# Kernel optimization log

Hardware: AMD Instinct MI355X
Metric: run time of the kernel (lower is better)

Reference implementation:

```python
import jax, jax.numpy as jnp
import numpy as np

B, T, C = 4, 2048, 2048
N_HEAD = 16
HEAD_DIM = C // N_HEAD  # 128
ROPE_BASE = 10000.0


def rope_cache(dim, seq_len, base=ROPE_BASE):
    inv_freq = 1.0 / (base ** (jnp.arange(0, dim, 2, dtype=jnp.float32) / dim))
    t = jnp.arange(seq_len, dtype=jnp.float32)
    freqs = jnp.outer(t, inv_freq)  # [T, dim//2]
    return jnp.cos(freqs), jnp.sin(freqs)


def apply_rope(q, k, cos, sin):
    # q, k: [B, H, T, D], interleaved-pair rotation
    q1, q2 = q[..., 0::2], q[..., 1::2]
    k1, k2 = k[..., 0::2], k[..., 1::2]
    c = cos[None, None, :, :]
    s = sin[None, None, :, :]
    q_rot = jnp.stack([q1 * c - q2 * s, q1 * s + q2 * c], axis=-1).reshape(q.shape)
    k_rot = jnp.stack([k1 * c - k2 * s, k1 * s + k2 * c], axis=-1).reshape(k.shape)
    return q_rot, k_rot


def setup_inputs() -> dict:
    key = jax.random.key(0)
    k1, k2, k3 = jax.random.split(key, 3)
    x = jax.random.normal(k1, (B, T, C), dtype=jnp.float32)
    W_attn = jax.random.normal(k2, (3 * C, C), dtype=jnp.float32) * (1.0 / np.sqrt(C))
    W_proj = jax.random.normal(k3, (C, C), dtype=jnp.float32) * (1.0 / np.sqrt(C))
    return {"x": x, "W_attn": W_attn, "W_proj": W_proj}


def reference(x, W_attn, W_proj):
    Bx, Tx, Cx = x.shape
    qkv = jnp.einsum('btc,fc->btf', x, W_attn)  # [B, T, 3C]
    q, k, v = jnp.split(qkv, 3, axis=-1)
    # [B, H, T, D]
    q = q.reshape(Bx, Tx, N_HEAD, HEAD_DIM).transpose(0, 2, 1, 3)
    k = k.reshape(Bx, Tx, N_HEAD, HEAD_DIM).transpose(0, 2, 1, 3)
    v = v.reshape(Bx, Tx, N_HEAD, HEAD_DIM).transpose(0, 2, 1, 3)
    cos, sin = rope_cache(HEAD_DIM, Tx)
    q, k = apply_rope(q, k, cos, sin)
    scale = 1.0 / np.sqrt(HEAD_DIM)
    scores = jnp.einsum('bhqd,bhkd->bhqk', q, k) * scale
    causal = jnp.tril(jnp.ones((Tx, Tx), dtype=bool))
    scores = jnp.where(causal[None, None, :, :], scores, jnp.finfo(scores.dtype).min)
    attn = jax.nn.softmax(scores, axis=-1)
    y = jnp.einsum('bhqk,bhkd->bhqd', attn, v)
    y = y.transpose(0, 2, 1, 3).reshape(Bx, Tx, Cx)
    return jnp.einsum('btc,fc->btf', y, W_proj)
```

## Files before the change

### kernel.cpp

```cpp
#include <hip/hip_runtime.h>
#include <stdint.h>

#define TT 2048
#define CC 2048
#define NHEAD 16
#define HD 128
#define NB 4
#define MTOT (NB*TT)
#define KD 2048
#define NT 32

typedef __attribute__((ext_vector_type(8))) short bf16x8;
typedef __attribute__((ext_vector_type(4))) float f32x4;
typedef __attribute__((ext_vector_type(16))) float f32x16;
typedef __attribute__((ext_vector_type(4))) unsigned u32x4;

__device__ __forceinline__ unsigned short f2bf(float f) {
  unsigned u = __float_as_uint(f);
  u += 0x7FFF + ((u >> 16) & 1);
  return (unsigned short)(u >> 16);
}
__device__ __forceinline__ float bf2f(unsigned short h) {
  return __uint_as_float(((unsigned)h) << 16);
}

__device__ __forceinline__ void gl_lds16(const unsigned short* g, short* l) {
  __builtin_amdgcn_global_load_lds(
      (const __attribute__((address_space(1))) void*)(g),
      (__attribute__((address_space(3))) void*)(l), 16, 0, 0);
}

#define MFMA16(a, b, c) __builtin_amdgcn_mfma_f32_16x16x32_bf16((a), (b), (c), 0, 0, 0)
#define MFMA32(a, b, c) __builtin_amdgcn_mfma_f32_32x32x16_bf16((a), (b), (c), 0, 0, 0)

#define PRE_MFMA() do { \
  __builtin_amdgcn_s_barrier(); \
  asm volatile("s_waitcnt lgkmcnt(0)" ::: "memory"); \
  __builtin_amdgcn_s_setprio(1); \
} while(0)
#define POST_MFMA() do { \
  __builtin_amdgcn_s_setprio(0); \
  __builtin_amdgcn_s_barrier(); \
  __builtin_amdgcn_sched_barrier(0); \
} while(0)

__global__ void k_f2b(const float* __restrict__ in, unsigned short* __restrict__ out, int n4) {
  int i = blockIdx.x * 256 + threadIdx.x;
  if (i >= n4) return;
  float4 v = reinterpret_cast<const float4*>(in)[i];
  ushort4 o;
  o.x = f2bf(v.x); o.y = f2bf(v.y); o.z = f2bf(v.z); o.w = f2bf(v.w);
  reinterpret_cast<ushort4*>(out)[i] = o;
}

__global__ void k_rope_tab(float* __restrict__ tab) {
  int t = blockIdx.x, i = threadIdx.x;
  double inv = exp2(-(double)i * (13.287712379549449062 / 64.0));
  double ang = (double)t * inv;
  tab[(t*64 + i)*2 + 0] = (float)cos(ang);
  tab[(t*64 + i)*2 + 1] = (float)sin(ang);
}

__device__ __forceinline__ void gemm256_core(
    const unsigned short* __restrict__ Ag,
    const unsigned short* __restrict__ Bg,
    int m0, int n0, short* lds, f32x4 (&acc)[8][4])
{
  const int tid = threadIdx.x;
  const int wid = tid >> 6, lane = tid & 63;
  const int wm = wid >> 2, wn = wid & 3;
  const int r15 = lane & 15, hi4 = lane >> 4;
  const int srow = wid*8 + (lane >> 3);
  const int schunk = (lane & 7) ^ (lane >> 3);

  const f32x4 fz = {0.f, 0.f, 0.f, 0.f};
#pragma unroll
  for (int i = 0; i < 8; i++)
#pragma unroll
    for (int j = 0; j < 4; j++) acc[i][j] = fz;

  int aoff0[8];
#pragma unroll
  for (int mi = 0; mi < 8; mi++) {
    int row = wm*128 + mi*16 + r15;
    aoff0[mi] = row*64 + ((hi4 ^ (row & 7))*8);
  }
  int boff0[4];
#pragma unroll
  for (int ni = 0; ni < 4; ni++) {
    int row = wn*64 + ni*16 + r15;
    boff0[ni] = row*64 + ((hi4 ^ (row & 7))*8);
  }

#define STAGE(G, L, GROW0, KT) do { \
    gl_lds16((G) + (size_t)((GROW0) + srow)*KD + (KT) + schunk*8, (L) + wid*512); \
    gl_lds16((G) + (size_t)((GROW0) + 64 + srow)*KD + (KT) + schunk*8, (L) + 4096 + wid*512); \
  } while(0)

  STAGE(Ag, lds,                        m0,       0);
  STAGE(Ag, lds + 8192,                 m0 + 128, 0);
  STAGE(Bg, lds + 32768,                n0,       0);
  STAGE(Bg, lds + 32768 + 8192,         n0 + 128, 0);
  STAGE(Bg, lds + 32768 + 16384,        n0,       64);
  STAGE(Bg, lds + 32768 + 16384 + 8192, n0 + 128, 64);
  asm volatile("s_waitcnt vmcnt(4)" ::: "memory");
  __builtin_amdgcn_s_barrier();
  __builtin_amdgcn_sched_barrier(0);

#pragma unroll 1
  for (int t = 0; t < NT; t++) {
    const int db = t & 1;
    short* Ab = lds + db*16384;
    short* Bb = lds + 32768 + db*16384;
    short* An = lds + (db ^ 1)*16384;
    const int kt = t*64;
    const bool stA = (t < NT - 1);
    const bool stB = (t < NT - 2);

    bf16x8 a[8], b[4][2];
#pragma unroll
    for (int mi = 0; mi < 8; mi++)
      a[mi] = *reinterpret_cast<const bf16x8*>(Ab + aoff0[mi]);
#pragma unroll
    for (int ni = 0; ni < 4; ni++) {
      b[ni][0] = *reinterpret_cast<const bf16x8*>(Bb + boff0[ni]);
      b[ni][1] = *reinterpret_cast<const bf16x8*>(Bb + (boff0[ni] ^ 32));
    }
    if (stA) {
      STAGE(Ag, An,        m0,       kt + 64);
      STAGE(Ag, An + 8192, m0 + 128, kt + 64);
    }
    PRE_MFMA();
#pragma unroll
    for (int mi = 0; mi < 8; mi++)
#pragma unroll
      for (int ni = 0; ni < 4; ni++)
        acc[mi][ni] = MFMA16(a[mi], b[ni][0], acc[mi][ni]);
    POST_MFMA();

#pragma unroll
    for (int mi = 0; mi < 8; mi++)
      a[mi] = *reinterpret_cast<const bf16x8*>(Ab + (aoff0[mi] ^ 32));
    if (stB) {
      STAGE(Bg, Bb,        n0,       kt + 128);
      STAGE(Bg, Bb + 8192, n0 + 128, kt + 128);
    }
    if (t >= NT - 2) asm volatile("s_waitcnt vmcnt(0)" ::: "memory");
    else             asm volatile("s_waitcnt vmcnt(4)" ::: "memory");
    PRE_MFMA();
#pragma unroll
    for (int mi = 0; mi < 8; mi++)
#pragma unroll
      for (int ni = 0; ni < 4; ni++)
        acc[mi][ni] = MFMA16(a[mi], b[ni][1], acc[mi][ni]);
    POST_MFMA();
  }
#undef STAGE
}

__global__ __launch_bounds__(512, 2) void k_qkv(
    const unsigned short* __restrict__ xb,
    const unsigned short* __restrict__ wab,
    unsigned short* __restrict__ qr,
    unsigned short* __restrict__ kr,
    unsigned short* __restrict__ vt)
{
  __shared__ __align__(16) short lds[65536];
  f32x4 acc[8][4];
  int bid = blockIdx.x;
  int swz = (bid & 7)*96 + (bid >> 3);
  int m0 = (swz / 24)*256, n0 = (swz % 24)*256;
  gemm256_core(xb, wab, m0, n0, lds, acc);

  int tid = threadIdx.x, wid = tid >> 6, lane = tid & 63;
  int wm = wid >> 2, wn = wid & 3, r15 = lane & 15, hi4 = lane >> 4;
  int nw0 = n0 + wn*64;
  int which = nw0 >> 11;
  int h = (nw0 & 2047) >> 7;
#pragma unroll
  for (int mi = 0; mi < 8; mi++) {
    int m_base = m0 + wm*128 + mi*16 + hi4*4;
    int b = m_base >> 11;
    int t0 = m_base & (TT - 1);
#pragma unroll
    for (int ni = 0; ni < 4; ni++) {
      int d = (nw0 & 127) + ni*16 + r15;
      if (which == 2) {
        ushort4 pv;
        pv.x = f2bf(acc[mi][ni][0]); pv.y = f2bf(acc[mi][ni][1]);
        pv.z = f2bf(acc[mi][ni][2]); pv.w = f2bf(acc[mi][ni][3]);
        *reinterpret_cast<ushort4*>(vt + ((size_t)((b*NHEAD + h)*HD + d))*TT + t0) = pv;
      } else {
        unsigned short* dst = (which == 0) ? qr : kr;
        size_t base = ((size_t)(b*NHEAD + h)*TT + t0)*HD + d;
#pragma unroll
        for (int r = 0; r < 4; r++) dst[base + (size_t)r*HD] = f2bf(acc[mi][ni][r]);
      }
    }
  }
}

__global__ __launch_bounds__(512, 2) void k_proj(
    const unsigned short* __restrict__ yb,
    const unsigned short* __restrict__ wpb,
    float* __restrict__ out)
{
  __shared__ __align__(16) short lds[65536];
  f32x4 acc[8][4];
  int bid = blockIdx.x;
  int swz = (bid & 7)*32 + (bid >> 3);
  int m0 = (swz / 8)*256, n0 = (swz % 8)*256;
  gemm256_core(yb, wpb, m0, n0, lds, acc);

  int tid = threadIdx.x, wid = tid >> 6, lane = tid & 63;
  int wm = wid >> 2, wn = wid & 3, r15 = lane & 15, hi4 = lane >> 4;
  int nw0 = n0 + wn*64;
#pragma unroll
  for (int mi = 0; mi < 8; mi++) {
    int m = m0 + wm*128 + mi*16 + hi4*4;
#pragma unroll
    for (int ni = 0; ni < 4; ni++) {
      int n = nw0 + ni*16 + r15;
#pragma unroll
      for (int r = 0; r < 4; r++)
        out[(size_t)(m + r)*CC + n] = acc[mi][ni][r];
    }
  }
}

__global__ void k_rope_apply(unsigned int* __restrict__ q32, unsigned int* __restrict__ k32,
                             const float* __restrict__ tab) {
  int i = blockIdx.x * 256 + threadIdx.x;
  int ii = i & 63;
  int t = (i >> 6) & (TT - 1);
  float c = tab[(t*64 + ii)*2], s = tab[(t*64 + ii)*2 + 1];
  unsigned qv = q32[i];
  float q1 = bf2f((unsigned short)qv), q2 = bf2f((unsigned short)(qv >> 16));
  unsigned short lo = f2bf(q1*c - q2*s), hi = f2bf(q1*s + q2*c);
  q32[i] = (unsigned)lo | ((unsigned)hi << 16);
  unsigned kv = k32[i];
  float k1 = bf2f((unsigned short)kv), k2 = bf2f((unsigned short)(kv >> 16));
  lo = f2bf(k1*c - k2*s); hi = f2bf(k1*s + k2*c);
  k32[i] = (unsigned)lo | ((unsigned)hi << 16);
}

__global__ __launch_bounds__(256, 1) void k_attn(
    const unsigned short* __restrict__ qr,
    const unsigned short* __restrict__ kr,
    const unsigned short* __restrict__ vt,
    unsigned short* __restrict__ yb)
{
  __shared__ __align__(16) short Ks[2][64*128];
  __shared__ __align__(16) short Vs[2][128*64];
  __shared__ float alds[4][32];
  int bid = blockIdx.x;
  int bh = bid & 63, pr = bid >> 6;
  int tid = threadIdx.x, w = tid >> 6, lane = tid & 63;
  int l31 = lane & 31, hi = lane >> 5;
  const unsigned short* qg = qr + (size_t)bh*TT*HD;
  const unsigned short* kg = kr + (size_t)bh*TT*HD;
  const unsigned short* vg = vt + (size_t)bh*HD*TT;
  const float scale = 0.08838834764831845f;
  int b = bh >> 4, h = bh & 15;

  int ksoff[4], vsoff[4];
#pragma unroll
  for (int i = 0; i < 4; i++) {
    int rK = (w*4 + i)*4 + (lane >> 4);
    int cK = (lane & 15) ^ (rK & 7);
    ksoff[i] = rK*HD + cK*8;
    int dV = (w*4 + i)*8 + (lane >> 3);
    int cV = (lane & 7) ^ (dV & 7);
    vsoff[i] = dV*TT + cV*8;
  }

#define STAGE_KV(BUF, KV0) do { \
    _Pragma("unroll") \
    for (int i_ = 0; i_ < 4; i_++) { \
      gl_lds16(kg + (size_t)(KV0)*HD + ksoff[i_], &Ks[BUF][(w*4 + i_)*512]); \
      gl_lds16(vg + (KV0) + vsoff[i_],            &Vs[BUF][(w*4 + i_)*512]); \
    } \
  } while(0)

#pragma unroll 1
  for (int ph = 0; ph < 2; ph++) {
    int qb = ph ? (15 - pr) : pr;
    int qlo = qb*128 + w*32;
    int qgi = qlo + l31;
    bf16x8 qf[8];
#pragma unroll
    for (int kk = 0; kk < 8; kk++)
      qf[kk] = *reinterpret_cast<const bf16x8*>(qg + (size_t)qgi*HD + kk*16 + hi*8);

    f32x16 ao[4];
#pragma unroll
    for (int dt = 0; dt < 4; dt++)
#pragma unroll
      for (int r = 0; r < 16; r++) ao[dt][r] = 0.f;
    float mrow = -3.0e38f, lsum = 0.f;
    int ntiles = 2*qb + 2;

    STAGE_KV(0, 0);
    __syncthreads();
    int cur = 0;

#pragma unroll 1
    for (int it = 0; it < ntiles; ++it) {
      int kv0 = it*64;
      if (it + 1 < ntiles) STAGE_KV(cur ^ 1, kv0 + 64);
      if (kv0 <= qlo + 31) {
        const short* Kc = Ks[cur];
        const short* Vc = Vs[cur];
        bool full = (kv0 + 63 <= qlo);
        f32x16 s0, s1;
#pragma unroll
        for (int r = 0; r < 16; r++) { s0[r] = 0.f; s1[r] = 0.f; }
        __builtin_amdgcn_s_setprio(1);
#pragma unroll
        for (int kk = 0; kk < 8; kk++) {
          int row0 = l31, row1 = 32 + l31;
          int ch0 = ((2*kk + hi) ^ (row0 & 7));
          int ch1 = ((2*kk + hi) ^ (row1 & 7));
          bf16x8 kf0 = *reinterpret_cast<const bf16x8*>((const char*)Kc + row0*256 + ch0*16);
          bf16x8 kf1 = *reinterpret_cast<const bf16x8*>((const char*)Kc + row1*256 + ch1*16);
          s0 = MFMA32(kf0, qf[kk], s0);
          s1 = MFMA32(kf1, qf[kk], s1);
        }
        __builtin_amdgcn_s_setprio(0);
        float p[32];
#pragma unroll
        for (int r = 0; r < 16; r++) {
          int kvl = (r & 3) + 8*(r >> 2) + 4*hi;
          float v0 = s0[r]*scale, v1 = s1[r]*scale;
          if (!full) {
            v0 = (kv0 + kvl      <= qgi) ? v0 : -3.0e38f;
            v1 = (kv0 + 32 + kvl <= qgi) ? v1 : -3.0e38f;
          }
          p[r] = v0; p[16 + r] = v1;
        }
        float t16[16];
#pragma unroll
        for (int i = 0; i < 16; i++) t16[i] = fmaxf(p[i], p[i + 16]);
#pragma unroll
        for (int i = 0; i < 8; i++) t16[i] = fmaxf(t16[i], t16[i + 8]);
#pragma unroll
        for (int i = 0; i < 4; i++) t16[i] = fmaxf(t16[i], t16[i + 4]);
        float mx = fmaxf(fmaxf(t16[0], t16[1]), fmaxf(t16[2], t16[3]));
        mx = fmaxf(mx, __shfl_xor(mx, 32));
        bool defer = __all(mx <= mrow + 8.f);
        if (!defer) {
          float mnew = fmaxf(mrow, mx);
          float alpha = __expf(mrow - mnew);
          mrow = mnew;
          lsum *= alpha;
          if (lane < 32) alds[w][lane] = alpha;
#pragma unroll
          for (int r = 0; r < 16; r++) {
            int ql = (r & 3) + 8*(r >> 2) + 4*hi;
            float av = alds[w][ql];
#pragma unroll
            for (int dt = 0; dt < 4; dt++) ao[dt][r] *= av;
          }
        }
#pragma unroll
        for (int i = 0; i < 32; i++) p[i] = __expf(p[i] - mrow);
#pragma unroll
        for (int i = 0; i < 16; i++) t16[i] = p[i] + p[i + 16];
#pragma unroll
        for (int i = 0; i < 8; i++) t16[i] = t16[i] + t16[i + 8];
#pragma unroll
        for (int i = 0; i < 4; i++) t16[i] = t16[i] + t16[i + 4];
        float rs = (t16[0] + t16[1]) + (t16[2] + t16[3]);
        rs += __shfl_xor(rs, 32);
        lsum += rs;
        bf16x8 pa[4];
#pragma unroll
        for (int ks = 0; ks < 4; ks++) {
          const int base = (ks >> 1)*16 + (ks & 1)*8;
          unsigned a0, a1, b0, b1;
          asm("v_cvt_pk_bf16_f32 %0, %1, %2" : "=v"(a0) : "v"(p[base + 0]), "v"(p[base + 1]));
          asm("v_cvt_pk_bf16_f32 %0, %1, %2" : "=v"(a1) : "v"(p[base + 2]), "v"(p[base + 3]));
          asm("v_cvt_pk_bf16_f32 %0, %1, %2" : "=v"(b0) : "v"(p[base + 4]), "v"(p[base + 5]));
          asm("v_cvt_pk_bf16_f32 %0, %1, %2" : "=v"(b1) : "v"(p[base + 6]), "v"(p[base + 7]));
          unsigned sa0 = (unsigned)__shfl_xor((int)a0, 32);
          unsigned sa1 = (unsigned)__shfl_xor((int)a1, 32);
          unsigned sb0 = (unsigned)__shfl_xor((int)b0, 32);
          unsigned sb1 = (unsigned)__shfl_xor((int)b1, 32);
          u32x4 pw;
          pw.x = hi ? sb0 : a0;
          pw.y = hi ? sb1 : a1;
          pw.z = hi ? b0 : sa0;
          pw.w = hi ? b1 : sa1;
          pa[ks] = __builtin_bit_cast(bf16x8, pw);
        }
        __builtin_amdgcn_s_setprio(1);
#pragma unroll
        for (int dt = 0; dt < 4; dt++) {
          int d = dt*32 + l31;
#pragma unroll
          for (int ks = 0; ks < 4; ks++) {
            int ch = ((2*ks + hi) ^ (d & 7));
            bf16x8 vf = *reinterpret_cast<const bf16x8*>((const char*)Vc + d*128 + ch*16);
            ao[dt] = MFMA32(pa[ks], vf, ao[dt]);
          }
        }
        __builtin_amdgcn_s_setprio(0);
      }
      __syncthreads();
      cur ^= 1;
    }
    if (lane < 32) alds[w][lane] = 1.0f / lsum;
#pragma unroll
    for (int r = 0; r < 16; r++) {
      int ql = (r & 3) + 8*(r >> 2) + 4*hi;
      float lv = alds[w][ql];
      int t = qlo + ql;
      size_t base = ((size_t)b*TT + t)*CC + h*HD + l31;
#pragma unroll
      for (int dt = 0; dt < 4; dt++)
        yb[base + dt*32] = f2bf(ao[dt][r] * lv);
    }
    __syncthreads();
  }
#undef STAGE_KV
}

extern "C" void kernel_launch(void* const* d_in, const int* in_sizes, int n_in,
                              void* d_out, int out_size, void* d_ws, size_t ws_size,
                              hipStream_t stream) {
  const float* x  = (const float*)d_in[0];
  const float* wa = (const float*)d_in[1];
  const float* wp = (const float*)d_in[2];
  float* out = (float*)d_out;
  char* ws = (char*)d_ws;
  size_t off = 0;
  unsigned short* xb  = (unsigned short*)(ws + off); off += (size_t)MTOT*CC*2;
  unsigned short* wab = (unsigned short*)(ws + off); off += (size_t)3*CC*CC*2;
  unsigned short* wpb = (unsigned short*)(ws + off); off += (size_t)CC*CC*2;
  unsigned short* qr  = (unsigned short*)(ws + off); off += (size_t)MTOT*CC*2;
  unsigned short* kr  = (unsigned short*)(ws + off); off += (size_t)MTOT*CC*2;
  unsigned short* vt  = (unsigned short*)(ws + off); off += (size_t)MTOT*CC*2;
  unsigned short* yb  = (unsigned short*)(ws + off); off += (size_t)MTOT*CC*2;
  float* tab          = (float*)(ws + off);          off += (size_t)TT*64*2*4;

  k_f2b<<<dim3(16384), dim3(256), 0, stream>>>(x,  xb,  MTOT*CC/4);
  k_f2b<<<dim3(12288), dim3(256), 0, stream>>>(wa, wab, 3*CC*CC/4);
  k_f2b<<<dim3(4096),  dim3(256), 0, stream>>>(wp, wpb, CC*CC/4);
  k_rope_tab<<<dim3(TT), dim3(64), 0, stream>>>(tab);
  k_qkv<<<dim3(768), dim3(512), 0, stream>>>(xb, wab, qr, kr, vt);
  k_rope_apply<<<dim3(32768), dim3(256), 0, stream>>>((unsigned int*)qr, (unsigned int*)kr, tab);
  k_attn<<<dim3(512), dim3(256), 0, stream>>>(qr, kr, vt, yb);
  k_proj<<<dim3(256), dim3(512), 0, stream>>>(yb, wpb, out);
}
```

Before: 485.5 us.

## Fuse RoPE into QKV GEMM epilogue and merge MFMA halves per K-tile

Removes the separate RoPE kernel: the QKV GEMM epilogue now rotates q/k pairs using a lane shuffle to fetch the partner element and reads cos/sin from the table before storing bf16. This drops a full read-modify-write pass over Q and K. Separately, the GEMM main loop loads both K-halves of A up front and issues all 64 MFMAs in one block, collapsing four barriers per iteration to two. That raises register pressure for the extra A fragments and changes the load/compute overlap, which could affect the 2-blocks-per-CU occupancy.

```diff
diff --git a/kernel.cpp b/kernel.cpp
--- a/kernel.cpp
+++ b/kernel.cpp
@@ -32,17 +32,6 @@
 
 #define MFMA16(a, b, c) __builtin_amdgcn_mfma_f32_16x16x32_bf16((a), (b), (c), 0, 0, 0)
 #define MFMA32(a, b, c) __builtin_amdgcn_mfma_f32_32x32x16_bf16((a), (b), (c), 0, 0, 0)
-
-#define PRE_MFMA() do { \
-  __builtin_amdgcn_s_barrier(); \
-  asm volatile("s_waitcnt lgkmcnt(0)" ::: "memory"); \
-  __builtin_amdgcn_s_setprio(1); \
-} while(0)
-#define POST_MFMA() do { \
-  __builtin_amdgcn_s_setprio(0); \
-  __builtin_amdgcn_s_barrier(); \
-  __builtin_amdgcn_sched_barrier(0); \
-} while(0)
 
 __global__ void k_f2b(const float* __restrict__ in, unsigned short* __restrict__ out, int n4) {
   int i = blockIdx.x * 256 + threadIdx.x;
@@ -114,46 +103,42 @@
     short* Bb = lds + 32768 + db*16384;
     short* An = lds + (db ^ 1)*16384;
     const int kt = t*64;
-    const bool stA = (t < NT - 1);
-    const bool stB = (t < NT - 2);
-
-    bf16x8 a[8], b[4][2];
-#pragma unroll
-    for (int mi = 0; mi < 8; mi++)
-      a[mi] = *reinterpret_cast<const bf16x8*>(Ab + aoff0[mi]);
+
+    bf16x8 a[8][2], b[4][2];
+#pragma unroll
+    for (int mi = 0; mi < 8; mi++) {
+      a[mi][0] = *reinterpret_cast<const bf16x8*>(Ab + aoff0[mi]);
+      a[mi][1] = *reinterpret_cast<const bf16x8*>(Ab + (aoff0[mi] ^ 32));
+    }
 #pragma unroll
     for (int ni = 0; ni < 4; ni++) {
       b[ni][0] = *reinterpret_cast<const bf16x8*>(Bb + boff0[ni]);
       b[ni][1] = *reinterpret_cast<const bf16x8*>(Bb + (boff0[ni] ^ 32));
     }
-    if (stA) {
+    if (t < NT - 1) {
       STAGE(Ag, An,        m0,       kt + 64);
       STAGE(Ag, An + 8192, m0 + 128, kt + 64);
     }
-    PRE_MFMA();
-#pragma unroll
-    for (int mi = 0; mi < 8; mi++)
-#pragma unroll
-      for (int ni = 0; ni < 4; ni++)
-        acc[mi][ni] = MFMA16(a[mi], b[ni][0], acc[mi][ni]);
-    POST_MFMA();
-
-#pragma unroll
-    for (int mi = 0; mi < 8; mi++)
-      a[mi] = *reinterpret_cast<const bf16x8*>(Ab + (aoff0[mi] ^ 32));
-    if (stB) {
+    __builtin_amdgcn_s_setprio(1);
+#pragma unroll
+    for (int kk = 0; kk < 2; kk++)
+#pragma unroll
+      for (int mi = 0; mi < 8; mi++)
+#pragma unroll
+        for (int ni = 0; ni < 4; ni++)
+          acc[mi][ni] = MFMA16(a[mi][kk], b[ni][kk], acc[mi][ni]);
+    __builtin_amdgcn_s_setprio(0);
+    asm volatile("s_waitcnt lgkmcnt(0)" ::: "memory");
+    __builtin_amdgcn_s_barrier();
+    __builtin_amdgcn_sched_barrier(0);
+    if (t < NT - 2) {
       STAGE(Bg, Bb,        n0,       kt + 128);
       STAGE(Bg, Bb + 8192, n0 + 128, kt + 128);
     }
     if (t >= NT - 2) asm volatile("s_waitcnt vmcnt(0)" ::: "memory");
     else             asm volatile("s_waitcnt vmcnt(4)" ::: "memory");
-    PRE_MFMA();
-#pragma unroll
-    for (int mi = 0; mi < 8; mi++)
-#pragma unroll
-      for (int ni = 0; ni < 4; ni++)
-        acc[mi][ni] = MFMA16(a[mi], b[ni][1], acc[mi][ni]);
-    POST_MFMA();
+    __builtin_amdgcn_s_barrier();
+    __builtin_amdgcn_sched_barrier(0);
   }
 #undef STAGE
 }
@@ -161,6 +146,7 @@
 __global__ __launch_bounds__(512, 2) void k_qkv(
     const unsigned short* __restrict__ xb,
     const unsigned short* __restrict__ wab,
+    const float* __restrict__ tab,
     unsigned short* __restrict__ qr,
     unsigned short* __restrict__ kr,
     unsigned short* __restrict__ vt)
@@ -193,8 +179,16 @@
       } else {
         unsigned short* dst = (which == 0) ? qr : kr;
         size_t base = ((size_t)(b*NHEAD + h)*TT + t0)*HD + d;
-#pragma unroll
-        for (int r = 0; r < 4; r++) dst[base + (size_t)r*HD] = f2bf(acc[mi][ni][r]);
+        int j = d >> 1;
+        bool odd = (d & 1);
+#pragma unroll
+        for (int r = 0; r < 4; r++) {
+          float v = acc[mi][ni][r];
+          float pv = __shfl_xor(v, 1);
+          float2 cs = *reinterpret_cast<const float2*>(tab + ((size_t)(t0 + r)*64 + j)*2);
+          float res = odd ? (pv*cs.y + v*cs.x) : (v*cs.x - pv*cs.y);
+          dst[base + (size_t)r*HD] = f2bf(res);
+        }
       }
     }
   }
@@ -226,22 +220,6 @@
         out[(size_t)(m + r)*CC + n] = acc[mi][ni][r];
     }
   }
-}
-
-__global__ void k_rope_apply(unsigned int* __restrict__ q32, unsigned int* __restrict__ k32,
-                             const float* __restrict__ tab) {
-  int i = blockIdx.x * 256 + threadIdx.x;
-  int ii = i & 63;
-  int t = (i >> 6) & (TT - 1);
-  float c = tab[(t*64 + ii)*2], s = tab[(t*64 + ii)*2 + 1];
-  unsigned qv = q32[i];
-  float q1 = bf2f((unsigned short)qv), q2 = bf2f((unsigned short)(qv >> 16));
-  unsigned short lo = f2bf(q1*c - q2*s), hi = f2bf(q1*s + q2*c);
-  q32[i] = (unsigned)lo | ((unsigned)hi << 16);
-  unsigned kv = k32[i];
-  float k1 = bf2f((unsigned short)kv), k2 = bf2f((unsigned short)(kv >> 16));
-  lo = f2bf(k1*c - k2*s); hi = f2bf(k1*s + k2*c);
-  k32[i] = (unsigned)lo | ((unsigned)hi << 16);
 }
 
 __global__ __launch_bounds__(256, 1) void k_attn(
@@ -447,8 +425,7 @@
   k_f2b<<<dim3(12288), dim3(256), 0, stream>>>(wa, wab, 3*CC*CC/4);
   k_f2b<<<dim3(4096),  dim3(256), 0, stream>>>(wp, wpb, CC*CC/4);
   k_rope_tab<<<dim3(TT), dim3(64), 0, stream>>>(tab);
-  k_qkv<<<dim3(768), dim3(512), 0, stream>>>(xb, wab, qr, kr, vt);
-  k_rope_apply<<<dim3(32768), dim3(256), 0, stream>>>((unsigned int*)qr, (unsigned int*)kr, tab);
+  k_qkv<<<dim3(768), dim3(512), 0, stream>>>(xb, wab, tab, qr, kr, vt);
   k_attn<<<dim3(512), dim3(256), 0, stream>>>(qr, kr, vt, yb);
   k_proj<<<dim3(256), dim3(512), 0, stream>>>(yb, wpb, out);
 }
```

After: 470.9 us. -3.0%, faster.

## Fuse RoPE into QKV epilogue and enlarge attention blocks to 8 waves

Applied to the files above, without the earlier changes.

Applies the rotary embedding inside the QKV GEMM epilogue, using a lane shuffle to fetch the paired element, and removes the separate rope-apply kernel that reread and rewrote all of Q and K. The attention kernel now runs 512 threads per block over 256-row query blocks with 256 blocks total, sharing each staged K/V tile across 8 waves. This halves the K/V global traffic per query row. It risks lower occupancy, coarser load balance across the causal pairing, and extra table loads and shuffles in the GEMM epilogue.

```diff
diff --git a/kernel.cpp b/kernel.cpp
--- a/kernel.cpp
+++ b/kernel.cpp
@@ -161,6 +161,7 @@
 __global__ __launch_bounds__(512, 2) void k_qkv(
     const unsigned short* __restrict__ xb,
     const unsigned short* __restrict__ wab,
+    const float* __restrict__ tab,
     unsigned short* __restrict__ qr,
     unsigned short* __restrict__ kr,
     unsigned short* __restrict__ vt)
@@ -193,8 +194,16 @@
       } else {
         unsigned short* dst = (which == 0) ? qr : kr;
         size_t base = ((size_t)(b*NHEAD + h)*TT + t0)*HD + d;
-#pragma unroll
-        for (int r = 0; r < 4; r++) dst[base + (size_t)r*HD] = f2bf(acc[mi][ni][r]);
+        int j = d >> 1;
+        bool odd = (d & 1);
+#pragma unroll
+        for (int r = 0; r < 4; r++) {
+          float v = acc[mi][ni][r];
+          float pv = __shfl_xor(v, 1);
+          float2 cs = *reinterpret_cast<const float2*>(tab + ((size_t)(t0 + r)*64 + j)*2);
+          float res = odd ? (pv*cs.y + v*cs.x) : (v*cs.x - pv*cs.y);
+          dst[base + (size_t)r*HD] = f2bf(res);
+        }
       }
     }
   }
@@ -228,23 +237,7 @@
   }
 }
 
-__global__ void k_rope_apply(unsigned int* __restrict__ q32, unsigned int* __restrict__ k32,
-                             const float* __restrict__ tab) {
-  int i = blockIdx.x * 256 + threadIdx.x;
-  int ii = i & 63;
-  int t = (i >> 6) & (TT - 1);
-  float c = tab[(t*64 + ii)*2], s = tab[(t*64 + ii)*2 + 1];
-  unsigned qv = q32[i];
-  float q1 = bf2f((unsigned short)qv), q2 = bf2f((unsigned short)(qv >> 16));
-  unsigned short lo = f2bf(q1*c - q2*s), hi = f2bf(q1*s + q2*c);
-  q32[i] = (unsigned)lo | ((unsigned)hi << 16);
-  unsigned kv = k32[i];
-  float k1 = bf2f((unsigned short)kv), k2 = bf2f((unsigned short)(kv >> 16));
-  lo = f2bf(k1*c - k2*s); hi = f2bf(k1*s + k2*c);
-  k32[i] = (unsigned)lo | ((unsigned)hi << 16);
-}
-
-__global__ __launch_bounds__(256, 1) void k_attn(
+__global__ __launch_bounds__(512, 1) void k_attn(
     const unsigned short* __restrict__ qr,
     const unsigned short* __restrict__ kr,
     const unsigned short* __restrict__ vt,
@@ -252,7 +245,7 @@
 {
   __shared__ __align__(16) short Ks[2][64*128];
   __shared__ __align__(16) short Vs[2][128*64];
-  __shared__ float alds[4][32];
+  __shared__ float alds[8][32];
   int bid = blockIdx.x;
   int bh = bid & 63, pr = bid >> 6;
   int tid = threadIdx.x, w = tid >> 6, lane = tid & 63;
@@ -263,29 +256,30 @@
   const float scale = 0.08838834764831845f;
   int b = bh >> 4, h = bh & 15;
 
-  int ksoff[4], vsoff[4];
-#pragma unroll
-  for (int i = 0; i < 4; i++) {
-    int rK = (w*4 + i)*4 + (lane >> 4);
+  int ksoff[2], vsoff[2];
+#pragma unroll
+  for (int i = 0; i < 2; i++) {
+    int c = w*2 + i;
+    int rK = c*4 + (lane >> 4);
     int cK = (lane & 15) ^ (rK & 7);
     ksoff[i] = rK*HD + cK*8;
-    int dV = (w*4 + i)*8 + (lane >> 3);
+    int dV = c*8 + (lane >> 3);
     int cV = (lane & 7) ^ (dV & 7);
     vsoff[i] = dV*TT + cV*8;
   }
 
 #define STAGE_KV(BUF, KV0) do { \
     _Pragma("unroll") \
-    for (int i_ = 0; i_ < 4; i_++) { \
-      gl_lds16(kg + (size_t)(KV0)*HD + ksoff[i_], &Ks[BUF][(w*4 + i_)*512]); \
-      gl_lds16(vg + (KV0) + vsoff[i_],            &Vs[BUF][(w*4 + i_)*512]); \
+    for (int i_ = 0; i_ < 2; i_++) { \
+      gl_lds16(kg + (size_t)(KV0)*HD + ksoff[i_], &Ks[BUF][(w*2 + i_)*512]); \
+      gl_lds16(vg + (KV0) + vsoff[i_],            &Vs[BUF][(w*2 + i_)*512]); \
     } \
   } while(0)
 
 #pragma unroll 1
   for (int ph = 0; ph < 2; ph++) {
-    int qb = ph ? (15 - pr) : pr;
-    int qlo = qb*128 + w*32;
+    int qb = ph ? (7 - pr) : pr;
+    int qlo = qb*256 + w*32;
     int qgi = qlo + l31;
     bf16x8 qf[8];
 #pragma unroll
@@ -298,7 +292,7 @@
 #pragma unroll
       for (int r = 0; r < 16; r++) ao[dt][r] = 0.f;
     float mrow = -3.0e38f, lsum = 0.f;
-    int ntiles = 2*qb + 2;
+    int ntiles = 4*qb + 4;
 
     STAGE_KV(0, 0);
     __syncthreads();
@@ -447,8 +441,7 @@
   k_f2b<<<dim3(12288), dim3(256), 0, stream>>>(wa, wab, 3*CC*CC/4);
   k_f2b<<<dim3(4096),  dim3(256), 0, stream>>>(wp, wpb, CC*CC/4);
   k_rope_tab<<<dim3(TT), dim3(64), 0, stream>>>(tab);
-  k_qkv<<<dim3(768), dim3(512), 0, stream>>>(xb, wab, qr, kr, vt);
-  k_rope_apply<<<dim3(32768), dim3(256), 0, stream>>>((unsigned int*)qr, (unsigned int*)kr, tab);
-  k_attn<<<dim3(512), dim3(256), 0, stream>>>(qr, kr, vt, yb);
+  k_qkv<<<dim3(768), dim3(512), 0, stream>>>(xb, wab, tab, qr, kr, vt);
+  k_attn<<<dim3(256), dim3(512), 0, stream>>>(qr, kr, vt, yb);
   k_proj<<<dim3(256), dim3(512), 0, stream>>>(yb, wpb, out);
 }
```

Result: faster. 411.0 us (-15.3%).
